# Kernel tuning notes

Hardware: AMD Instinct MI355X
Metric: run time of the kernel (lower is better)

## Reference

```python
import jax, jax.numpy as jnp
import numpy as np

N, E, D, L, G = 10000, 320000, 256, 5, 128
RWSE, DEG_V = 16, 1001
BN_EPS = 1e-5


def setup_inputs() -> dict:
    key = jax.random.key(0)
    ks = jax.random.split(key, 12)
    s = 1.0 / np.sqrt(D)
    return {
        'feat_id': jax.random.randint(ks[0], (N,), 0, 100000, dtype=jnp.int64 if jax.config.jax_enable_x64 else jnp.int32),
        'edge_index': jax.random.randint(ks[1], (2, E), 0, N),
        'batch_idx': jnp.sort(jax.random.randint(ks[2], (N,), 0, G)),
        'rwse': jax.random.normal(ks[3], (N, RWSE), jnp.float32),
        'in_degrees': jax.random.randint(ks[4], (N,), 0, DEG_V),
        # value_projection: Linear(fixed_input_dim=D -> D); stored as [in, out]
        'w_val': jax.random.normal(ks[5], (D, D), jnp.float32) * s,
        'b_val': jnp.zeros((D,), jnp.float32),
        # rwse_projection: Linear(RWSE -> D)
        'w_rwse': jax.random.normal(ks[6], (RWSE, D), jnp.float32) * (1.0 / np.sqrt(RWSE)),
        'b_rwse': jnp.zeros((D,), jnp.float32),
        # degree_embedding table (clamped to [0, 1000])
        'deg_emb': jax.random.normal(ks[7], (DEG_V, D), jnp.float32) * 0.02,
        # per-layer GIN MLP: Linear-ReLU-Linear, stacked over L layers
        'mlp_w1': jax.random.normal(ks[8], (L, D, D), jnp.float32) * s,
        'mlp_b1': jnp.zeros((L, D), jnp.float32),
        'mlp_w2': jax.random.normal(ks[9], (L, D, D), jnp.float32) * s,
        'mlp_b2': jnp.zeros((L, D), jnp.float32),
        # BatchNorm1d (eval mode: running stats)
        'bn_gamma': jnp.ones((L, D), jnp.float32),
        'bn_beta': jnp.zeros((L, D), jnp.float32),
        'bn_mean': jnp.zeros((L, D), jnp.float32),
        'bn_var': jax.random.uniform(ks[10], (L, D), jnp.float32, 0.5, 1.5),
        # GIN eps per layer
        'eps_gin': jnp.zeros((L,), jnp.float32),
    }


def reference(feat_id, edge_index, batch_idx, rwse, in_degrees,
              w_val, b_val, w_rwse, b_rwse, deg_emb,
              mlp_w1, mlp_b1, mlp_w2, mlp_b2,
              bn_gamma, bn_beta, bn_mean, bn_var, eps_gin):
    # --- node feature embedding ---
    h_id = jnp.remainder(feat_id, D)
    h_one = jax.nn.one_hot(h_id, D, dtype=jnp.float32)            # [N, D]
    h = h_one @ w_val + b_val + rwse @ w_rwse + b_rwse            # value + rwse projections
    deg = jnp.clip(in_degrees, 0, 1000)
    h = h + deg_emb[deg]                                          # degree embedding

    src, dst = edge_index[0], edge_index[1]
    for l in range(L):
        # GIN message passing: sum neighbor features into dst (gather -> scatter-add)
        agg = jax.ops.segment_sum(h[src], dst, num_segments=N)    # [N, D]
        y = agg + (1.0 + eps_gin[l]) * h
        # MLP (Linear-ReLU-Linear)
        y = jax.nn.relu(y @ mlp_w1[l] + mlp_b1[l]) @ mlp_w2[l] + mlp_b2[l]
        # BatchNorm1d (eval: running stats) + ReLU
        y = (y - bn_mean[l]) * (bn_gamma[l] * jax.lax.rsqrt(bn_var[l] + BN_EPS)) + bn_beta[l]
        h = jax.nn.relu(y)

    # --- mean pooling per graph ---
    sums = jax.ops.segment_sum(h, batch_idx, num_segments=G)                     # [G, D]
    cnt = jax.ops.segment_sum(jnp.ones((N, 1), h.dtype), batch_idx, num_segments=G)
    graph_feature = sums / jnp.maximum(cnt, 1.0)
    return graph_feature, h
```

## Files before the change

### kernel.cpp

```cpp
#include <hip/hip_runtime.h>
#include <hip/hip_bf16.h>

#define N_NODES 10000
#define N_EDGES 320000
#define DIM     256
#define N_LAYERS 5
#define N_GRAPHS 128
#define RWSE_K  16
#define GBM 16

typedef __bf16 bf16_t;
typedef bf16_t bf16x8 __attribute__((ext_vector_type(8)));
typedef float  f32x4  __attribute__((ext_vector_type(4)));

__device__ inline ushort f2bf(float f) {
    union { float f; unsigned u; } v; v.f = f;
    unsigned r = v.u + 0x7fff + ((v.u >> 16) & 1);
    return (ushort)(r >> 16);
}
__device__ inline float bfbits2f(unsigned hi16) {
    union { unsigned u; float f; } v; v.u = hi16;
    return v.f;
}

__global__ __launch_bounds__(256)
void setup_kernel(const int* __restrict__ feat_id,
                  const float* __restrict__ rwse,
                  const int* __restrict__ in_deg,
                  const float* __restrict__ w_val,
                  const float* __restrict__ b_val,
                  const float* __restrict__ w_rwse,
                  const float* __restrict__ b_rwse,
                  const float* __restrict__ deg_emb,
                  ushort* __restrict__ hb,
                  const int* __restrict__ ei, int* __restrict__ cnt_arr,
                  const float* __restrict__ w1, const float* __restrict__ w2,
                  ushort* __restrict__ wt1, ushort* __restrict__ wt2,
                  const float* __restrict__ gamma, const float* __restrict__ beta,
                  const float* __restrict__ mean, const float* __restrict__ var,
                  const float* __restrict__ b2, float* __restrict__ scale,
                  float* __restrict__ shift,
                  const int* __restrict__ batch, float* __restrict__ invcnt) {
    __shared__ float r[RWSE_K];
    __shared__ float t[32][33];
    int b = blockIdx.x;
    int tid = threadIdx.x;
    if (b < N_NODES) {
        int i = b, d = tid;
        if (d < RWSE_K) r[d] = rwse[i * RWSE_K + d];
        __syncthreads();
        int hid = feat_id[i] & (DIM - 1);
        int dg = in_deg[i];
        dg = dg < 0 ? 0 : (dg > 1000 ? 1000 : dg);
        float v = w_val[hid * DIM + d] + b_val[d] + b_rwse[d] + deg_emb[dg * DIM + d];
#pragma unroll
        for (int k = 0; k < RWSE_K; ++k) v += r[k] * w_rwse[k * DIM + d];
        hb[i * DIM + d] = f2bf(v);
    } else if (b < 11250) {
        int e = (b - N_NODES) * 256 + tid;
        if (e < N_EDGES) atomicAdd(&cnt_arr[ei[N_EDGES + e]], 1);
    } else if (b < 11890) {
        int w_id = b - 11250;
        int l = w_id >> 7;
        int rem = w_id & 127;
        int mat = rem >> 6;
        int tile = rem & 63;
        const float* W  = (mat ? w2  : w1)  + (size_t)l * DIM * DIM;
        ushort*      Wt = (mat ? wt2 : wt1) + (size_t)l * DIM * DIM;
        int k0 = (tile >> 3) * 32, n0 = (tile & 7) * 32;
        int tx = tid & 31, ty = tid >> 5;
#pragma unroll
        for (int j = 0; j < 4; ++j)
            t[ty + j * 8][tx] = W[(k0 + ty + j * 8) * DIM + n0 + tx];
        __syncthreads();
#pragma unroll
        for (int j = 0; j < 4; ++j)
            Wt[(n0 + ty + j * 8) * DIM + k0 + tx] = f2bf(t[tx][ty + j * 8]);
    } else if (b < 11895) {
        int l = b - 11890;
        int idx = l * DIM + tid;
        float s = gamma[idx] * rsqrtf(var[idx] + 1e-5f);
        scale[idx] = s;
        shift[idx] = beta[idx] + (b2[idx] - mean[idx]) * s;
    } else {
        int g = tid;
        if (g < N_GRAPHS) {
            int l = 0, rr = N_NODES;
            while (l < rr) { int m = (l + rr) >> 1; if (batch[m] < g) l = m + 1; else rr = m; }
            int lo = l;
            rr = N_NODES;
            while (l < rr) { int m = (l + rr) >> 1; if (batch[m] < g + 1) l = m + 1; else rr = m; }
            int c = l - lo;
            invcnt[g] = 1.0f / (float)(c < 1 ? 1 : c);
        }
    }
}

__global__ __launch_bounds__(1024)
void scan_kernel(const int* __restrict__ cnt_arr, int* __restrict__ cur, int n) {
    __shared__ int wsum[16];
    __shared__ int carry_sh;
    int tid = threadIdx.x, wave = tid >> 6, lane = tid & 63;
    if (tid == 0) carry_sh = 0;
    __syncthreads();
    for (int base = 0; base < n; base += 1024) {
        int idx = base + tid;
        int v = (idx < n) ? cnt_arr[idx] : 0;
        int s = v;
#pragma unroll
        for (int off = 1; off < 64; off <<= 1) {
            int t = __shfl_up(s, off, 64);
            if (lane >= off) s += t;
        }
        if (lane == 63) wsum[wave] = s;
        __syncthreads();
        if (wave == 0) {
            int ws = (lane < 16) ? wsum[lane] : 0;
#pragma unroll
            for (int off = 1; off < 16; off <<= 1) {
                int t = __shfl_up(ws, off, 64);
                if (lane >= off) ws += t;
            }
            if (lane < 16) wsum[lane] = ws;
        }
        __syncthreads();
        int excl = s - v + (wave ? wsum[wave - 1] : 0) + carry_sh;
        if (idx < n) cur[idx] = excl;
        __syncthreads();
        if (tid == 0) carry_sh += wsum[15];
        __syncthreads();
    }
}

__global__ __launch_bounds__(256)
void fill_kernel(const int* __restrict__ ei, int* __restrict__ cur,
                 int* __restrict__ cs) {
    int e = blockIdx.x * 256 + threadIdx.x;
    if (e < N_EDGES) {
        int d = ei[N_EDGES + e];
        int p = atomicAdd(&cur[d], 1);
        cs[p] = ei[e];
    }
}

#define ACCV(v)                                                        \
    acc[0] += bfbits2f((v).x << 16); acc[1] += bfbits2f((v).x & 0xffff0000u); \
    acc[2] += bfbits2f((v).y << 16); acc[3] += bfbits2f((v).y & 0xffff0000u); \
    acc[4] += bfbits2f((v).z << 16); acc[5] += bfbits2f((v).z & 0xffff0000u); \
    acc[6] += bfbits2f((v).w << 16); acc[7] += bfbits2f((v).w & 0xffff0000u);

__global__ __launch_bounds__(256)
void layer_kernel(const ushort* __restrict__ hb_in,
                  const int* __restrict__ cur, const int* __restrict__ cs,
                  const float* __restrict__ eps_gin, int layer,
                  const ushort* __restrict__ Wt1, const float* __restrict__ b1,
                  const ushort* __restrict__ Wt2,
                  const float* __restrict__ bnsc, const float* __restrict__ bnsh,
                  float* __restrict__ outF, ushort* __restrict__ outB,
                  const int* __restrict__ batch, const float* __restrict__ invcnt,
                  float* __restrict__ poolOut) {
    __shared__ __align__(16) ushort As[GBM][DIM + 8];
    __shared__ __align__(16) ushort Bs[DIM][72];
    __shared__ int   g_sh[GBM];
    __shared__ float sc_sh[GBM];
    int tx = threadIdx.x;
    int row0 = blockIdx.x * GBM;
    int wave = tx >> 6, lane = tx & 63, quad = lane >> 4, l16 = lane & 15;
    int half = lane >> 5, sl = lane & 31;
    int wc = wave * 64;
    int srow2 = tx >> 3;
    int skol2 = (tx & 7) * 8;
    const uint4* hb4 = (const uint4*)hb_in;
    float sc = 1.0f + eps_gin[layer];

    if (poolOut && tx < GBM) {
        int gg = batch[row0 + tx];
        g_sh[tx] = gg;
        sc_sh[tx] = invcnt[gg];
    }

#pragma unroll
    for (int n = 0; n < 4; ++n) {
        int r = wave * 4 + n;
        int i = row0 + r;
        float acc[8];
#pragma unroll
        for (int t = 0; t < 8; ++t) acc[t] = 0.f;
        int e0 = i ? cur[i - 1] : 0;
        int e1 = cur[i];
        for (int base = e0; base < e1; base += 64) {
            int rem = e1 - base;
            int cnt = rem < 64 ? rem : 64;
            int idx = (base + lane < e1) ? cs[base + lane] : 0;
            int j = 0;
            for (; j + 8 <= cnt; j += 8) {
                int s0 = __shfl(idx, j + half, 64);
                int s1 = __shfl(idx, j + 2 + half, 64);
                int s2 = __shfl(idx, j + 4 + half, 64);
                int s3 = __shfl(idx, j + 6 + half, 64);
                uint4 v0 = hb4[(size_t)s0 * 32 + sl];
                uint4 v1 = hb4[(size_t)s1 * 32 + sl];
                uint4 v2 = hb4[(size_t)s2 * 32 + sl];
                uint4 v3 = hb4[(size_t)s3 * 32 + sl];
                ACCV(v0); ACCV(v1); ACCV(v2); ACCV(v3);
            }
            for (; j + 2 <= cnt; j += 2) {
                int s = __shfl(idx, j + half, 64);
                uint4 v = hb4[(size_t)s * 32 + sl];
                ACCV(v);
            }
            if (j < cnt) {
                int s = __shfl(idx, j, 64);
                if (half == 0) {
                    uint4 v = hb4[(size_t)s * 32 + sl];
                    ACCV(v);
                }
            }
        }
#pragma unroll
        for (int t = 0; t < 8; ++t) acc[t] += __shfl_xor(acc[t], 32, 64);
        if (half == 0) {
            uint4 sv = hb4[(size_t)i * 32 + sl];
            acc[0] += bfbits2f(sv.x << 16) * sc; acc[1] += bfbits2f(sv.x & 0xffff0000u) * sc;
            acc[2] += bfbits2f(sv.y << 16) * sc; acc[3] += bfbits2f(sv.y & 0xffff0000u) * sc;
            acc[4] += bfbits2f(sv.z << 16) * sc; acc[5] += bfbits2f(sv.z & 0xffff0000u) * sc;
            acc[6] += bfbits2f(sv.w << 16) * sc; acc[7] += bfbits2f(sv.w & 0xffff0000u) * sc;
            uint4 o;
            o.x = (uint)f2bf(acc[0]) | ((uint)f2bf(acc[1]) << 16);
            o.y = (uint)f2bf(acc[2]) | ((uint)f2bf(acc[3]) << 16);
            o.z = (uint)f2bf(acc[4]) | ((uint)f2bf(acc[5]) << 16);
            o.w = (uint)f2bf(acc[6]) | ((uint)f2bf(acc[7]) << 16);
            *(uint4*)&As[r][sl * 8] = o;
        }
    }
    __syncthreads();

    f32x4 acc4[4];
#pragma unroll
    for (int t = 0; t < 4; ++t) acc4[t] = (f32x4){0.f, 0.f, 0.f, 0.f};
    for (int k0 = 0; k0 < DIM; k0 += 64) {
#pragma unroll
        for (int j = 0; j < 8; ++j) {
            int rr = srow2 + 32 * j;
            *(uint4*)&Bs[rr][skol2] = *(const uint4*)&Wt1[(size_t)rr * DIM + k0 + skol2];
        }
        __syncthreads();
#pragma unroll
        for (int kk = 0; kk < 2; ++kk) {
            bf16x8 af = *(const bf16x8*)&As[l16][k0 + kk * 32 + quad * 8];
#pragma unroll
            for (int tj = 0; tj < 4; ++tj) {
                bf16x8 bfv = *(const bf16x8*)&Bs[wc + tj * 16 + l16][kk * 32 + quad * 8];
                acc4[tj] = __builtin_amdgcn_mfma_f32_16x16x32_bf16(af, bfv, acc4[tj], 0, 0, 0);
            }
        }
        __syncthreads();
    }
#pragma unroll
    for (int tj = 0; tj < 4; ++tj) {
        int col = wc + tj * 16 + l16;
        float bias = b1[col];
#pragma unroll
        for (int r = 0; r < 4; ++r)
            As[quad * 4 + r][col] = f2bf(fmaxf(acc4[tj][r] + bias, 0.f));
    }
    __syncthreads();

#pragma unroll
    for (int t = 0; t < 4; ++t) acc4[t] = (f32x4){0.f, 0.f, 0.f, 0.f};
    for (int k0 = 0; k0 < DIM; k0 += 64) {
#pragma unroll
        for (int j = 0; j < 8; ++j) {
            int rr = srow2 + 32 * j;
            *(uint4*)&Bs[rr][skol2] = *(const uint4*)&Wt2[(size_t)rr * DIM + k0 + skol2];
        }
        __syncthreads();
#pragma unroll
        for (int kk = 0; kk < 2; ++kk) {
            bf16x8 af = *(const bf16x8*)&As[l16][k0 + kk * 32 + quad * 8];
#pragma unroll
            for (int tj = 0; tj < 4; ++tj) {
                bf16x8 bfv = *(const bf16x8*)&Bs[wc + tj * 16 + l16][kk * 32 + quad * 8];
                acc4[tj] = __builtin_amdgcn_mfma_f32_16x16x32_bf16(af, bfv, acc4[tj], 0, 0, 0);
            }
        }
        __syncthreads();
    }
    float* Pf = (float*)&Bs[0][0];
#pragma unroll
    for (int tj = 0; tj < 4; ++tj) {
        int col = wc + tj * 16 + l16;
        float s = bnsc[col], sh = bnsh[col];
#pragma unroll
        for (int r = 0; r < 4; ++r) {
            int row = row0 + quad * 4 + r;
            float v = fmaxf(acc4[tj][r] * s + sh, 0.f);
            if (outF) outF[(size_t)row * DIM + col] = v;
            if (outB) outB[(size_t)row * DIM + col] = f2bf(v);
            if (poolOut) Pf[(quad * 4 + r) * 260 + col] = v * sc_sh[quad * 4 + r];
        }
    }
    if (poolOut) {
        __syncthreads();
        int gcur = g_sh[0];
        float ssum = 0.f;
#pragma unroll
        for (int rr = 0; rr < GBM; ++rr) {
            if (g_sh[rr] != gcur) {
                atomicAdd(&poolOut[(size_t)gcur * DIM + tx], ssum);
                gcur = g_sh[rr];
                ssum = 0.f;
            }
            ssum += Pf[rr * 260 + tx];
        }
        atomicAdd(&poolOut[(size_t)gcur * DIM + tx], ssum);
    }
}

extern "C" void kernel_launch(void* const* d_in, const int* in_sizes, int n_in,
                              void* d_out, int out_size, void* d_ws, size_t ws_size,
                              hipStream_t stream) {
    const int*   feat_id  = (const int*)d_in[0];
    const int*   ei       = (const int*)d_in[1];
    const int*   batch    = (const int*)d_in[2];
    const float* rwse     = (const float*)d_in[3];
    const int*   in_deg   = (const int*)d_in[4];
    const float* w_val    = (const float*)d_in[5];
    const float* b_val    = (const float*)d_in[6];
    const float* w_rwse   = (const float*)d_in[7];
    const float* b_rwse   = (const float*)d_in[8];
    const float* deg_emb  = (const float*)d_in[9];
    const float* mlp_w1   = (const float*)d_in[10];
    const float* mlp_b1   = (const float*)d_in[11];
    const float* mlp_w2   = (const float*)d_in[12];
    const float* mlp_b2   = (const float*)d_in[13];
    const float* bn_gamma = (const float*)d_in[14];
    const float* bn_beta  = (const float*)d_in[15];
    const float* bn_mean  = (const float*)d_in[16];
    const float* bn_var   = (const float*)d_in[17];
    const float* eps_gin  = (const float*)d_in[18];

    float* out = (float*)d_out;
    float* out_h = out + N_GRAPHS * DIM;

    char* w = (char*)d_ws;
    ushort* hb0  = (ushort*)w;
    ushort* hb1  = hb0 + (size_t)N_NODES * DIM;
    ushort* wt1  = hb1 + (size_t)N_NODES * DIM;
    ushort* wt2  = wt1 + (size_t)N_LAYERS * DIM * DIM;
    int* cnt_arr = (int*)(wt2 + (size_t)N_LAYERS * DIM * DIM);
    int* cur     = cnt_arr + N_NODES;
    int* cs      = cur + N_NODES;
    float* bnsc  = (float*)(cs + N_EDGES);
    float* bnsh  = bnsc + N_LAYERS * DIM;
    float* invcnt = bnsh + N_LAYERS * DIM;

    hipMemsetAsync(cnt_arr, 0, N_NODES * sizeof(int), stream);

    setup_kernel<<<11896, 256, 0, stream>>>(
        feat_id, rwse, in_deg, w_val, b_val, w_rwse, b_rwse, deg_emb,
        hb0, ei, cnt_arr, mlp_w1, mlp_w2, wt1, wt2,
        bn_gamma, bn_beta, bn_mean, bn_var, mlp_b2, bnsc, bnsh,
        batch, invcnt);
    scan_kernel<<<1, 1024, 0, stream>>>(cnt_arr, cur, N_NODES);
    fill_kernel<<<(N_EDGES + 255) / 256, 256, 0, stream>>>(ei, cur, cs);

    int ggrid = N_NODES / GBM;
    for (int l = 0; l < N_LAYERS; ++l) {
        bool last = (l == N_LAYERS - 1);
        const ushort* hin = (l & 1) ? hb1 : hb0;
        ushort* hout = (l & 1) ? hb0 : hb1;
        layer_kernel<<<ggrid, 256, 0, stream>>>(
            hin, cur, cs, eps_gin, l,
            wt1 + (size_t)l * DIM * DIM, mlp_b1 + l * DIM,
            wt2 + (size_t)l * DIM * DIM, bnsc + l * DIM, bnsh + l * DIM,
            last ? out_h : nullptr, last ? nullptr : hout,
            batch, invcnt, last ? out : nullptr);
    }
}
```

Before: 314.9 us.

## Fuse five GIN layer launches into one cooperative kernel with grid sync

Moves the per-layer body into a device function and runs all five layers inside one persistent cooperative kernel, using grid.sync between layers instead of separate launches. It targets launch overhead and the inter-kernel gaps between layers. It needs all 625 blocks to be co-resident (checked once via an occupancy query), and a grid-wide barrier costs something of its own. It falls back to per-layer launches when cooperative launch is unavailable.

```diff
diff --git a/kernel.cpp b/kernel.cpp
--- a/kernel.cpp
+++ b/kernel.cpp
@@ -1,5 +1,8 @@
 #include <hip/hip_runtime.h>
 #include <hip/hip_bf16.h>
+#include <hip/hip_cooperative_groups.h>
+
+namespace cg = cooperative_groups;
 
 #define N_NODES 10000
 #define N_EDGES 320000
@@ -8,6 +11,7 @@
 #define N_GRAPHS 128
 #define RWSE_K  16
 #define GBM 16
+#define GRID 625
 
 typedef __bf16 bf16_t;
 typedef bf16_t bf16x8 __attribute__((ext_vector_type(8)));
@@ -149,20 +153,17 @@
     acc[4] += bfbits2f((v).z << 16); acc[5] += bfbits2f((v).z & 0xffff0000u); \
     acc[6] += bfbits2f((v).w << 16); acc[7] += bfbits2f((v).w & 0xffff0000u);
 
-__global__ __launch_bounds__(256)
-void layer_kernel(const ushort* __restrict__ hb_in,
-                  const int* __restrict__ cur, const int* __restrict__ cs,
-                  const float* __restrict__ eps_gin, int layer,
-                  const ushort* __restrict__ Wt1, const float* __restrict__ b1,
-                  const ushort* __restrict__ Wt2,
-                  const float* __restrict__ bnsc, const float* __restrict__ bnsh,
-                  float* __restrict__ outF, ushort* __restrict__ outB,
-                  const int* __restrict__ batch, const float* __restrict__ invcnt,
-                  float* __restrict__ poolOut) {
-    __shared__ __align__(16) ushort As[GBM][DIM + 8];
-    __shared__ __align__(16) ushort Bs[DIM][72];
-    __shared__ int   g_sh[GBM];
-    __shared__ float sc_sh[GBM];
+__device__ __forceinline__ void layer_body(
+        const ushort* __restrict__ hb_in,
+        const int* __restrict__ cur, const int* __restrict__ cs,
+        const float* __restrict__ eps_gin, int layer,
+        const ushort* __restrict__ Wt1, const float* __restrict__ b1,
+        const ushort* __restrict__ Wt2,
+        const float* __restrict__ bnsc, const float* __restrict__ bnsh,
+        float* __restrict__ outF, ushort* __restrict__ outB,
+        const int* __restrict__ batch, const float* __restrict__ invcnt,
+        float* __restrict__ poolOut,
+        ushort (*As)[DIM + 8], ushort (*Bs)[72], int* g_sh, float* sc_sh) {
     int tx = threadIdx.x;
     int row0 = blockIdx.x * GBM;
     int wave = tx >> 6, lane = tx & 63, quad = lane >> 4, l16 = lane & 15;
@@ -314,6 +315,54 @@
             ssum += Pf[rr * 260 + tx];
         }
         atomicAdd(&poolOut[(size_t)gcur * DIM + tx], ssum);
+    }
+}
+
+__global__ __launch_bounds__(256)
+void layer_kernel(const ushort* __restrict__ hb_in,
+                  const int* __restrict__ cur, const int* __restrict__ cs,
+                  const float* __restrict__ eps_gin, int layer,
+                  const ushort* __restrict__ Wt1, const float* __restrict__ b1,
+                  const ushort* __restrict__ Wt2,
+                  const float* __restrict__ bnsc, const float* __restrict__ bnsh,
+                  float* __restrict__ outF, ushort* __restrict__ outB,
+                  const int* __restrict__ batch, const float* __restrict__ invcnt,
+                  float* __restrict__ poolOut) {
+    __shared__ __align__(16) ushort As[GBM][DIM + 8];
+    __shared__ __align__(16) ushort Bs[DIM][72];
+    __shared__ int   g_sh[GBM];
+    __shared__ float sc_sh[GBM];
+    layer_body(hb_in, cur, cs, eps_gin, layer, Wt1, b1, Wt2, bnsc, bnsh,
+               outF, outB, batch, invcnt, poolOut, As, Bs, g_sh, sc_sh);
+}
+
+struct LP {
+    const int* batch; const float* eps_gin; const float* mlp_b1;
+    ushort* hb0; ushort* hb1; ushort* wt1; ushort* wt2;
+    int* cur; int* cs;
+    float* bnsc; float* bnsh; float* invcnt;
+    float* out; float* out_h;
+};
+
+__global__ __launch_bounds__(256)
+void layers_coop(LP p) {
+    cg::grid_group grid = cg::this_grid();
+    __shared__ __align__(16) ushort As[GBM][DIM + 8];
+    __shared__ __align__(16) ushort Bs[DIM][72];
+    __shared__ int   g_sh[GBM];
+    __shared__ float sc_sh[GBM];
+    for (int l = 0; l < N_LAYERS; ++l) {
+        if (l) { __threadfence(); grid.sync(); }
+        bool last = (l == N_LAYERS - 1);
+        const ushort* hin = (l & 1) ? p.hb1 : p.hb0;
+        ushort* houtB = last ? nullptr : ((l & 1) ? p.hb0 : p.hb1);
+        layer_body(hin, p.cur, p.cs, p.eps_gin, l,
+                   p.wt1 + (size_t)l * DIM * DIM, p.mlp_b1 + l * DIM,
+                   p.wt2 + (size_t)l * DIM * DIM,
+                   p.bnsc + l * DIM, p.bnsh + l * DIM,
+                   last ? p.out_h : nullptr, houtB,
+                   p.batch, p.invcnt, last ? p.out : nullptr,
+                   As, Bs, g_sh, sc_sh);
     }
 }
 
@@ -365,16 +414,41 @@
     scan_kernel<<<1, 1024, 0, stream>>>(cnt_arr, cur, N_NODES);
     fill_kernel<<<(N_EDGES + 255) / 256, 256, 0, stream>>>(ei, cur, cs);
 
-    int ggrid = N_NODES / GBM;
-    for (int l = 0; l < N_LAYERS; ++l) {
-        bool last = (l == N_LAYERS - 1);
-        const ushort* hin = (l & 1) ? hb1 : hb0;
-        ushort* hout = (l & 1) ? hb0 : hb1;
-        layer_kernel<<<ggrid, 256, 0, stream>>>(
-            hin, cur, cs, eps_gin, l,
-            wt1 + (size_t)l * DIM * DIM, mlp_b1 + l * DIM,
-            wt2 + (size_t)l * DIM * DIM, bnsc + l * DIM, bnsh + l * DIM,
-            last ? out_h : nullptr, last ? nullptr : hout,
-            batch, invcnt, last ? out : nullptr);
-    }
-}
+    static int coop_state = -1;
+    if (coop_state == -1) {
+        int nb = 0;
+        hipError_t e1 = hipOccupancyMaxActiveBlocksPerMultiprocessor(
+            &nb, layers_coop, 256, 0);
+        hipDeviceProp_t prop;
+        hipError_t e2 = hipGetDeviceProperties(&prop, 0);
+        coop_state = (e1 == hipSuccess && e2 == hipSuccess &&
+                      (long)nb * prop.multiProcessorCount >= GRID) ? 1 : 0;
+    }
+
+    LP lp;
+    lp.batch = batch; lp.eps_gin = eps_gin; lp.mlp_b1 = mlp_b1;
+    lp.hb0 = hb0; lp.hb1 = hb1; lp.wt1 = wt1; lp.wt2 = wt2;
+    lp.cur = cur; lp.cs = cs;
+    lp.bnsc = bnsc; lp.bnsh = bnsh; lp.invcnt = invcnt;
+    lp.out = out; lp.out_h = out_h;
+
+    bool coop_done = false;
+    if (coop_state == 1) {
+        void* kargs[] = { (void*)&lp };
+        coop_done = (hipLaunchCooperativeKernel((const void*)layers_coop,
+                        dim3(GRID), dim3(256), kargs, 0, stream) == hipSuccess);
+    }
+    if (!coop_done) {
+        for (int l = 0; l < N_LAYERS; ++l) {
+            bool last = (l == N_LAYERS - 1);
+            const ushort* hin = (l & 1) ? hb1 : hb0;
+            ushort* hout = (l & 1) ? hb0 : hb1;
+            layer_kernel<<<GRID, 256, 0, stream>>>(
+                hin, cur, cs, eps_gin, l,
+                wt1 + (size_t)l * DIM * DIM, mlp_b1 + l * DIM,
+                wt2 + (size_t)l * DIM * DIM, bnsc + l * DIM, bnsh + l * DIM,
+                last ? out_h : nullptr, last ? nullptr : hout,
+                batch, invcnt, last ? out : nullptr);
+        }
+    }
+}
```

Result: no change. 315.0 us (+0.0%).
